# Optimization experiments

Measured on AMD Instinct MI355X. Metric: run time of the kernel, lower is better.

Reference implementation:

```python
import jax, jax.numpy as jnp
import numpy as np

D_MODEL = 1024
N_HEADS = 16
HEAD = D_MODEL // N_HEADS  # 64
D_FF = 4096
LN_EPS = 1e-5


def _layernorm(x, g, b):
    mu = jnp.mean(x, axis=-1, keepdims=True)
    var = jnp.mean(jnp.square(x - mu), axis=-1, keepdims=True)
    return (x - mu) * jax.lax.rsqrt(var + LN_EPS) * g + b


def _mha(q_in, k_in, v_in, Wq, Wk, Wv, bv, causal):
    # Wq/Wk/Wv: [H, d_model, head]; bv: [H, head] (value proj has bias, q/k do not)
    q = jnp.einsum('bsd,hde->bhse', q_in, Wq)
    k = jnp.einsum('btd,hde->bhte', k_in, Wk)
    v = jnp.einsum('btd,hde->bhte', v_in, Wv) + bv[None, :, None, :]
    scale = HEAD ** -0.5
    scores = jnp.einsum('bhse,bhte->bhst', q, k) * scale
    if causal:
        S, T = scores.shape[-2], scores.shape[-1]
        mask = jnp.tril(jnp.ones((S, T), dtype=bool))
        scores = jnp.where(mask, scores, -jnp.inf)
    p = jax.nn.softmax(scores, axis=-1)
    o = jnp.einsum('bhst,bhte->bhse', p, v)  # [B,H,S,head]
    B, H, S, E = o.shape
    return o.transpose(0, 2, 1, 3).reshape(B, S, H * E)  # concat heads in order


def setup_inputs() -> dict:
    key = jax.random.key(0)
    ks = jax.random.split(key, 20)
    B, S, T = 2, 2048, 2048
    sd = D_MODEL ** -0.5
    inp = {
        'input_tensor': jax.random.normal(ks[0], (B, S, D_MODEL), jnp.float32),
        'encoder_output': jax.random.normal(ks[1], (B, T, D_MODEL), jnp.float32),
        # masked self-attention params
        'Wq1': jax.random.normal(ks[2], (N_HEADS, D_MODEL, HEAD), jnp.float32) * sd,
        'Wk1': jax.random.normal(ks[3], (N_HEADS, D_MODEL, HEAD), jnp.float32) * sd,
        'Wv1': jax.random.normal(ks[4], (N_HEADS, D_MODEL, HEAD), jnp.float32) * sd,
        'bv1': jnp.zeros((N_HEADS, HEAD), jnp.float32),
        # cross-attention params
        'Wq2': jax.random.normal(ks[5], (N_HEADS, D_MODEL, HEAD), jnp.float32) * sd,
        'Wk2': jax.random.normal(ks[6], (N_HEADS, D_MODEL, HEAD), jnp.float32) * sd,
        'Wv2': jax.random.normal(ks[7], (N_HEADS, D_MODEL, HEAD), jnp.float32) * sd,
        'bv2': jnp.zeros((N_HEADS, HEAD), jnp.float32),
        # layernorms
        'g1': jnp.ones((D_MODEL,), jnp.float32), 'be1': jnp.zeros((D_MODEL,), jnp.float32),
        'g2': jnp.ones((D_MODEL,), jnp.float32), 'be2': jnp.zeros((D_MODEL,), jnp.float32),
        'g3': jnp.ones((D_MODEL,), jnp.float32), 'be3': jnp.zeros((D_MODEL,), jnp.float32),
        # FFN
        'Wf1': jax.random.normal(ks[8], (D_MODEL, D_FF), jnp.float32) * sd,
        'bf1': jnp.zeros((D_FF,), jnp.float32),
        'Wf2': jax.random.normal(ks[9], (D_FF, D_MODEL), jnp.float32) * (D_FF ** -0.5),
        'bf2': jnp.zeros((D_MODEL,), jnp.float32),
    }
    return inp


def reference(input_tensor, encoder_output, Wq1, Wk1, Wv1, bv1, Wq2, Wk2, Wv2, bv2,
              g1, be1, g2, be2, g3, be3, Wf1, bf1, Wf2, bf2):
    x = input_tensor
    # masked (causal) self-attention; dropout is identity in eval
    sa = _mha(x, x, x, Wq1, Wk1, Wv1, bv1, causal=True)
    x = _layernorm(sa + input_tensor, g1, be1)
    # cross-attention with encoder output (no mask)
    ca = _mha(x, encoder_output, encoder_output, Wq2, Wk2, Wv2, bv2, causal=False)
    x = _layernorm(x + ca, g2, be2)
    # FFN
    ffn = jax.nn.relu(x @ Wf1 + bf1) @ Wf2 + bf2
    x = _layernorm(x + ffn, g3, be3)
    return x
```

## Files before the change

kernel.cpp:

```cpp
#include <hip/hip_runtime.h>
#include <stdint.h>
#include <stddef.h>
#include <type_traits>

typedef __attribute__((ext_vector_type(8))) short short8;
typedef __attribute__((ext_vector_type(4))) short short4_t;
typedef __attribute__((ext_vector_type(4))) float float4_t;
typedef __attribute__((ext_vector_type(4))) unsigned uint4_t;

#define DEV static __device__ __forceinline__

#define QSCALE 0.18033688011112042f

DEV short f2bf(float f) {
  unsigned u = __builtin_bit_cast(unsigned, f);
  u = (u + 0x7FFFu + ((u >> 16) & 1u)) >> 16;
  return (short)(unsigned short)u;
}

DEV void load_lds16(const short* g, short* l) {
  __builtin_amdgcn_global_load_lds((const __attribute__((address_space(1))) void*)g,
                                   (__attribute__((address_space(3))) void*)l,
                                   16, 0, 0);
}

__global__ __launch_bounds__(256) void transpose_cvt(const float* __restrict__ src,
                                                     short* __restrict__ dst,
                                                     int R, int C) {
  __shared__ float t[64][65];
  src += (size_t)blockIdx.z * R * C;
  dst += (size_t)blockIdx.z * R * C;
  const int tid = threadIdx.x;
  const int r0 = blockIdx.y * 64, c0 = blockIdx.x * 64;
#pragma unroll
  for (int i = 0; i < 16; i++) {
    int r = i * 4 + (tid >> 6);
    t[r][tid & 63] = src[(size_t)(r0 + r) * C + c0 + (tid & 63)];
  }
  __syncthreads();
#pragma unroll
  for (int i = 0; i < 16; i++) {
    int c = i * 4 + (tid >> 6);
    dst[(size_t)(c0 + c) * R + r0 + (tid & 63)] = f2bf(t[tid & 63][c]);
  }
}

struct Repack6 {
  const float* src[6];
  short* dst[6];
};
__global__ __launch_bounds__(256) void transpose_cvt6(Repack6 a) {
  __shared__ float t[64][65];
  const int mat = blockIdx.z >> 4;
  const int head = blockIdx.z & 15;
  const float* src = a.src[mat] + (size_t)head * 1024 * 64;
  short* dst = a.dst[mat] + (size_t)head * 64 * 1024;
  const int tid = threadIdx.x;
  const int r0 = blockIdx.y * 64;
#pragma unroll
  for (int i = 0; i < 16; i++) {
    int r = i * 4 + (tid >> 6);
    t[r][tid & 63] = src[(size_t)(r0 + r) * 64 + (tid & 63)];
  }
  __syncthreads();
#pragma unroll
  for (int i = 0; i < 16; i++) {
    int c = i * 4 + (tid >> 6);
    dst[(size_t)c * 1024 + r0 + (tid & 63)] = f2bf(t[tid & 63][c]);
  }
}

__global__ __launch_bounds__(256) void cvt_bf16_2(const float* __restrict__ inA,
                                                  short* __restrict__ outA,
                                                  const float* __restrict__ inB,
                                                  short* __restrict__ outB, int n4) {
  int i = blockIdx.x * 256 + threadIdx.x;
  const float* in = blockIdx.z ? inB : inA;
  short* out = blockIdx.z ? outB : outA;
  if (i < n4) {
    float4_t v = ((const float4_t*)in)[i];
    short4_t o;
    o.x = f2bf(v.x); o.y = f2bf(v.y); o.z = f2bf(v.z); o.w = f2bf(v.w);
    ((short4_t*)out)[i] = o;
  }
}

struct GemmArgs {
  const short* A;
  const short* Bt;
  int M, N, K;
  float* outf;
  short* outb;
  short* Qo;
  short* Ko;
  short* Vt;
  const float* bias;
};

template <int MODE>
DEV void scatter1(const GemmArgs& args, int row, int col, float v) {
  if constexpr (MODE == 0) {
    int sel = col >> 10, cc = col & 1023;
    int h = cc >> 6, e = cc & 63;
    int b_ = row >> 11, s = row & 2047;
    if (sel == 0)
      args.Qo[(((size_t)(b_ * 16 + h)) * 2048 + s) * 64 + e] = f2bf(v * QSCALE);
    else if (sel == 1)
      args.Ko[(((size_t)(b_ * 16 + h)) * 2048 + s) * 64 + e] = f2bf(v);
    else {
      v += args.bias[cc];
      args.Vt[(((size_t)(b_ * 16 + h)) * 64 + e) * 2048 + s] = f2bf(v);
    }
  } else if constexpr (MODE == 1) {
    int h = col >> 6, e = col & 63;
    int b_ = row >> 11, s = row & 2047;
    args.Qo[(((size_t)(b_ * 16 + h)) * 2048 + s) * 64 + e] = f2bf(v * QSCALE);
  } else if constexpr (MODE == 2) {
    int sel = col >> 10, cc = col & 1023;
    int h = cc >> 6, e = cc & 63;
    int b_ = row >> 11, s = row & 2047;
    if (sel == 0)
      args.Ko[(((size_t)(b_ * 16 + h)) * 2048 + s) * 64 + e] = f2bf(v);
    else {
      v += args.bias[cc];
      args.Vt[(((size_t)(b_ * 16 + h)) * 64 + e) * 2048 + s] = f2bf(v);
    }
  } else if constexpr (MODE == 3) {
    v += args.bias[col];
    v = v > 0.f ? v : 0.f;
    args.outb[(size_t)row * args.N + col] = f2bf(v);
  } else {
    v += args.bias[col];
    args.outf[(size_t)row * args.N + col] = v;
  }
}

template <int MODE>
__global__ __launch_bounds__(256) void gemm_k(GemmArgs args) {
  constexpr int BM = 128, BK = 64;
  __shared__ short As[2][BM * BK];
  __shared__ short Bs[2][BM * BK];
  const int tid = threadIdx.x;
  const int lane = tid & 63;
  const int w = tid >> 6;
  const int wr = w >> 1, wc = w & 1;

  const int nwgx = gridDim.x;
  const int nxy = nwgx * gridDim.y;
  const int nwg = nxy * gridDim.z;
  const int orig = (blockIdx.z * gridDim.y + blockIdx.y) * nwgx + blockIdx.x;
  const int q8 = nwg >> 3;
  const int swz = (orig & 7) * q8 + (orig >> 3);
  const int zsl = swz / nxy;
  const int xy = swz % nxy;
  const int row0 = (xy / nwgx) * BM;
  const int col0 = (xy % nwgx) * BM;

  const int K = args.K;
  const int kLen = K / gridDim.z;
  const int kbase = zsl * kLen;
  const short* Ab = args.A + (size_t)row0 * K;
  const short* Bb = args.Bt + (size_t)col0 * K;
  float4_t acc[4][4] = {};
  const int r = lane & 15, kg = lane >> 4, rx = r & 7;

  auto stage = [&](int buf, int k0) {
#pragma unroll
    for (int i = 0; i < 4; i++) {
      int c = i * 256 + tid;
      int rw = c >> 3, sc = (c & 7) ^ (rw & 7);
      load_lds16(Ab + (size_t)rw * K + k0 + sc * 8, &As[buf][c * 8]);
    }
#pragma unroll
    for (int i = 0; i < 4; i++) {
      int c = i * 256 + tid;
      int rw = c >> 3, sc = (c & 7) ^ (rw & 7);
      load_lds16(Bb + (size_t)rw * K + k0 + sc * 8, &Bs[buf][c * 8]);
    }
  };

  stage(0, kbase);
  __syncthreads();
  int buf = 0;
  const int nk = kLen / BK;
  for (int t = 0; t < nk; t++) {
    if (t + 1 < nk) stage(buf ^ 1, kbase + (t + 1) * BK);
#pragma unroll
    for (int kk = 0; kk < BK; kk += 32) {
      const int ch = kk >> 3;
      short8 a[4], b[4];
#pragma unroll
      for (int m = 0; m < 4; m++)
        a[m] = *(const short8*)&As[buf][(wr * 64 + m * 16 + r) * BK + ((ch + kg) ^ rx) * 8];
#pragma unroll
      for (int n = 0; n < 4; n++)
        b[n] = *(const short8*)&Bs[buf][(wc * 64 + n * 16 + r) * BK + ((ch + kg) ^ rx) * 8];
#pragma unroll
      for (int m = 0; m < 4; m++)
#pragma unroll
        for (int n = 0; n < 4; n++)
          acc[m][n] = __builtin_amdgcn_mfma_f32_16x16x32_bf16(a[m], b[n], acc[m][n], 0, 0, 0);
    }
    __syncthreads();
    buf ^= 1;
  }

  float* dst5 = args.outf + (size_t)zsl * args.M * args.N;
#pragma unroll
  for (int m = 0; m < 4; m++)
#pragma unroll
    for (int n = 0; n < 4; n++)
#pragma unroll
      for (int j = 0; j < 4; j++) {
        int row = row0 + wr * 64 + m * 16 + kg * 4 + j;
        int col = col0 + wc * 64 + n * 16 + r;
        if constexpr (MODE == 5)
          dst5[(size_t)row * args.N + col] = acc[m][n][j];
        else
          scatter1<MODE>(args, row, col, acc[m][n][j]);
      }
}

template <int MODE>
__global__ __launch_bounds__(512, 2) void gemm256_k(GemmArgs args) {
  extern __shared__ short lds[];
  const int tid = threadIdx.x;
  const int lane = tid & 63;
  const int w = tid >> 6;
  const int wr = w >> 2, wc = w & 3;

  const int nwgx = gridDim.x;
  const int nwg = nwgx * gridDim.y;
  const int orig = blockIdx.y * nwgx + blockIdx.x;
  const int q8 = nwg >> 3;
  const int swz = (orig & 7) * q8 + (orig >> 3);
  const int row0 = (swz / nwgx) * 256;
  const int col0 = (swz % nwgx) * 256;

  const int K = args.K;
  const short* Ab = args.A + (size_t)row0 * K;
  const short* Bb = args.Bt + (size_t)col0 * K;
  const int r = lane & 15, kg = lane >> 4, rx = r & 7;
  float4_t acc[8][4] = {};

  auto stage = [&](int buf, int k0) {
    short* Ad = lds + buf * 16384;
    short* Bd = lds + 32768 + buf * 16384;
#pragma unroll
    for (int i = 0; i < 4; i++) {
      int c = i * 512 + tid;
      int rw = c >> 3, sc = (c & 7) ^ (rw & 7);
      load_lds16(Ab + (size_t)rw * K + k0 + sc * 8, Ad + c * 8);
    }
#pragma unroll
    for (int i = 0; i < 4; i++) {
      int c = i * 512 + tid;
      int rw = c >> 3, sc = (c & 7) ^ (rw & 7);
      load_lds16(Bb + (size_t)rw * K + k0 + sc * 8, Bd + c * 8);
    }
  };

  stage(0, 0);
  __syncthreads();
  int buf = 0;
  const int nk = K / 64;
  for (int t = 0; t < nk; t++) {
    if (t + 1 < nk) stage(buf ^ 1, (t + 1) * 64);
    const short* Ar = lds + buf * 16384;
    const short* Br = lds + 32768 + buf * 16384;
#pragma unroll
    for (int kk = 0; kk < 64; kk += 32) {
      const int ch = kk >> 3;
      short8 a[8], b[4];
#pragma unroll
      for (int m = 0; m < 8; m++)
        a[m] = *(const short8*)&Ar[(wr * 128 + m * 16 + r) * 64 + ((ch + kg) ^ rx) * 8];
#pragma unroll
      for (int n = 0; n < 4; n++)
        b[n] = *(const short8*)&Br[(wc * 64 + n * 16 + r) * 64 + ((ch + kg) ^ rx) * 8];
#pragma unroll
      for (int m = 0; m < 8; m++)
#pragma unroll
        for (int n = 0; n < 4; n++)
          acc[m][n] = __builtin_amdgcn_mfma_f32_16x16x32_bf16(a[m], b[n], acc[m][n], 0, 0, 0);
    }
    __syncthreads();
    buf ^= 1;
  }

#pragma unroll
  for (int m = 0; m < 8; m++)
#pragma unroll
    for (int n = 0; n < 4; n++)
#pragma unroll
      for (int j = 0; j < 4; j++)
        scatter1<MODE>(args, row0 + wr * 128 + m * 16 + kg * 4 + j,
                       col0 + wc * 64 + n * 16 + r, acc[m][n][j]);
}

template <bool CAUSAL>
__global__ __launch_bounds__(256) void attn_k(const short* __restrict__ Q,
                                              const short* __restrict__ Kq,
                                              const short* __restrict__ Vt,
                                              float* __restrict__ Out) {
  __shared__ short kst[2][64 * 64];
  __shared__ short vst[2][64 * 64];
  __shared__ unsigned p_lds[4][32 * 32];
  const int tid = threadIdx.x;
  const int lane = tid & 63;
  const int w = tid >> 6;
  const int bh = blockIdx.y;
  const int b_ = bh >> 4, h = bh & 15;
  const int qb = (blockIdx.x + blockIdx.y) & 15;
  const int qt = (blockIdx.y & 16) ? (15 - qb) : qb;
  const int q0w = qt * 128 + w * 32;
  const int r = lane & 15, kg = lane >> 4;
  const int rx = r & 7;
  const size_t base = (size_t)bh * 2048 * 64;
  const short* Qb = Q + base;
  const short* Kb = Kq + base;
  const short* Vb = Vt + base;

  short8 q[2][2];
#pragma unroll
  for (int qg = 0; qg < 2; qg++)
#pragma unroll
    for (int half = 0; half < 2; half++)
      q[qg][half] = *(const short8*)&Qb[(size_t)(q0w + qg * 16 + r) * 64 + half * 32 + kg * 8];

  float4_t o[2][4] = {};
  float lp[2] = {0.f, 0.f};

  const int NT = CAUSAL ? 2 * qt + 2 : 32;
  const float4_t zero4 = {0.f, 0.f, 0.f, 0.f};

  const int c0 = tid, c1 = tid + 256;
  const int row0s = c0 >> 3, cc0 = (c0 & 7) ^ (row0s & 7);
  const int row1s = c1 >> 3, cc1 = (c1 & 7) ^ (row1s & 7);

  auto stage = [&](int buf, int kt) {
    const short* ktk = Kb + (size_t)kt * 64 * 64;
    const short* ktv = Vb + (size_t)kt * 64;
    load_lds16(ktk + row0s * 64 + cc0 * 8, &kst[buf][c0 * 8]);
    load_lds16(ktk + row1s * 64 + cc1 * 8, &kst[buf][c1 * 8]);
    load_lds16(ktv + (size_t)row0s * 2048 + cc0 * 8, &vst[buf][c0 * 8]);
    load_lds16(ktv + (size_t)row1s * 2048 + cc1 * 8, &vst[buf][c1 * 8]);
  };

  auto body = [&](auto BUFC, int kt) {
    constexpr int BUF = decltype(BUFC)::value;
    short8 kb[4][2];
#pragma unroll
    for (int grp = 0; grp < 4; grp++)
#pragma unroll
      for (int half = 0; half < 2; half++)
        kb[grp][half] = *(const short8*)&kst[BUF][(grp * 16 + r) * 64 + ((half * 4 + kg) ^ rx) * 8];

    unsigned* p32 = &p_lds[w][0];
#pragma unroll
    for (int qg = 0; qg < 2; qg++) {
      float4_t sc[4];
      __builtin_amdgcn_s_setprio(1);
#pragma unroll
      for (int grp = 0; grp < 4; grp++) {
        float4_t t0 = __builtin_amdgcn_mfma_f32_16x16x32_bf16(kb[grp][0], q[qg][0], zero4, 0, 0, 0);
        sc[grp] = __builtin_amdgcn_mfma_f32_16x16x32_bf16(kb[grp][1], q[qg][1], t0, 0, 0, 0);
      }
      __builtin_amdgcn_s_setprio(0);

      float s[16];
#pragma unroll
      for (int grp = 0; grp < 4; grp++)
#pragma unroll
        for (int j = 0; j < 4; j++) s[grp * 4 + j] = sc[grp][j];

      if (CAUSAL && kt >= 2 * qt) {
        const int qrow = q0w + qg * 16 + r;
#pragma unroll
        for (int grp = 0; grp < 4; grp++)
#pragma unroll
          for (int j = 0; j < 4; j++)
            if (kt * 64 + grp * 16 + kg * 4 + j > qrow) s[grp * 4 + j] = -1e30f;
      }

      float p[16];
      float ps = 0.f;
#pragma unroll
      for (int i = 0; i < 16; i++) {
        p[i] = __builtin_amdgcn_exp2f(s[i]);
        ps += p[i];
      }
      lp[qg] += ps;

#pragma unroll
      for (int grp = 0; grp < 4; grp++) {
        unsigned pk01, pk23;
        asm("v_cvt_pk_bf16_f32 %0, %1, %2" : "=v"(pk01) : "v"(p[grp * 4 + 0]), "v"(p[grp * 4 + 1]));
        asm("v_cvt_pk_bf16_f32 %0, %1, %2" : "=v"(pk23) : "v"(p[grp * 4 + 2]), "v"(p[grp * 4 + 3]));
        int idx = (qg * 16 + r) * 32 + ((2 * grp + (kg >> 1)) ^ rx) * 4 + (kg & 1) * 2;
        p32[idx] = pk01;
        p32[idx + 1] = pk23;
      }
    }
    __builtin_amdgcn_sched_barrier(0);

    short8 pa[2][2];
#pragma unroll
    for (int qg = 0; qg < 2; qg++)
#pragma unroll
      for (int half = 0; half < 2; half++) {
        const int db = (qg * 16 + r) * 32 + ((half * 4 + kg) ^ rx) * 4;
        uint4_t t;
        t.x = p32[db + 0];
        t.y = p32[db + 1];
        t.z = p32[db + 2];
        t.w = p32[db + 3];
        pa[qg][half] = __builtin_bit_cast(short8, t);
      }

    __builtin_amdgcn_s_setprio(1);
#pragma unroll
    for (int n = 0; n < 4; n++) {
      short8 v0 = *(const short8*)&vst[BUF][(n * 16 + r) * 64 + ((0 * 4 + kg) ^ rx) * 8];
      short8 v1 = *(const short8*)&vst[BUF][(n * 16 + r) * 64 + ((1 * 4 + kg) ^ rx) * 8];
#pragma unroll
      for (int qg = 0; qg < 2; qg++) {
        o[qg][n] = __builtin_amdgcn_mfma_f32_16x16x32_bf16(v0, pa[qg][0], o[qg][n], 0, 0, 0);
        o[qg][n] = __builtin_amdgcn_mfma_f32_16x16x32_bf16(v1, pa[qg][1], o[qg][n], 0, 0, 0);
      }
    }
    __builtin_amdgcn_s_setprio(0);
  };

  stage(0, 0);
  __syncthreads();

  for (int kt = 0; kt < NT; kt += 2) {
    if (kt + 1 < NT) stage(1, kt + 1);
    body(std::integral_constant<int, 0>{}, kt);
    __syncthreads();
    if (kt + 1 >= NT) break;
    if (kt + 2 < NT) stage(0, kt + 2);
    body(std::integral_constant<int, 1>{}, kt + 1);
    __syncthreads();
  }

#pragma unroll
  for (int qg = 0; qg < 2; qg++) {
    float l = lp[qg];
    l += __shfl_xor(l, 16);
    l += __shfl_xor(l, 32);
    const float inv = 1.0f / l;
    float* orow = Out + ((size_t)b_ * 2048 + q0w + qg * 16 + r) * 1024 + h * 64;
#pragma unroll
    for (int n = 0; n < 4; n++)
#pragma unroll
      for (int j = 0; j < 4; j++)
        orow[n * 16 + kg * 4 + j] = o[qg][n][j] * inv;
  }
}

__global__ __launch_bounds__(256) void add_ln_k(const float* __restrict__ X,
                                                const float* __restrict__ Y,
                                                const float* __restrict__ g,
                                                const float* __restrict__ be,
                                                float* __restrict__ outf,
                                                short* __restrict__ outb) {
  __shared__ float red[8];
  const int row = blockIdx.x;
  const int t = threadIdx.x;
  const int lane = t & 63, w = t >> 6;
  float4_t v = ((const float4_t*)(X + (size_t)row * 1024))[t];
  float4_t u = ((const float4_t*)(Y + (size_t)row * 1024))[t];
  v.x += u.x; v.y += u.y; v.z += u.z; v.w += u.w;
  float s = v.x + v.y + v.z + v.w;
#pragma unroll
  for (int off = 32; off >= 1; off >>= 1) s += __shfl_xor(s, off);
  if (lane == 0) red[w] = s;
  __syncthreads();
  float mean = (red[0] + red[1] + red[2] + red[3]) * (1.f / 1024.f);
  float dx = v.x - mean, dy = v.y - mean, dz = v.z - mean, dw = v.w - mean;
  float q2 = dx * dx + dy * dy + dz * dz + dw * dw;
#pragma unroll
  for (int off = 32; off >= 1; off >>= 1) q2 += __shfl_xor(q2, off);
  if (lane == 0) red[4 + w] = q2;
  __syncthreads();
  float var = (red[4] + red[5] + red[6] + red[7]) * (1.f / 1024.f);
  float rs = rsqrtf(var + 1e-5f);
  float4_t gg = ((const float4_t*)g)[t];
  float4_t bb = ((const float4_t*)be)[t];
  float4_t o;
  o.x = dx * rs * gg.x + bb.x;
  o.y = dy * rs * gg.y + bb.y;
  o.z = dz * rs * gg.z + bb.z;
  o.w = dw * rs * gg.w + bb.w;
  ((float4_t*)(outf + (size_t)row * 1024))[t] = o;
  if (outb != nullptr) {
    short4_t ob;
    ob.x = f2bf(o.x); ob.y = f2bf(o.y); ob.z = f2bf(o.z); ob.w = f2bf(o.w);
    ((short4_t*)(outb + (size_t)row * 1024))[t] = ob;
  }
}

__global__ __launch_bounds__(256) void add_ln2_k(const float* __restrict__ X,
                                                 const float* __restrict__ P0,
                                                 const float* __restrict__ P1,
                                                 const float* __restrict__ bias,
                                                 const float* __restrict__ g,
                                                 const float* __restrict__ be,
                                                 float* __restrict__ outf) {
  __shared__ float red[8];
  const int row = blockIdx.x;
  const int t = threadIdx.x;
  const int lane = t & 63, w = t >> 6;
  float4_t v = ((const float4_t*)(X + (size_t)row * 1024))[t];
  float4_t u0 = ((const float4_t*)(P0 + (size_t)row * 1024))[t];
  float4_t u1 = ((const float4_t*)(P1 + (size_t)row * 1024))[t];
  float4_t bi = ((const float4_t*)bias)[t];
  v.x += u0.x + u1.x + bi.x;
  v.y += u0.y + u1.y + bi.y;
  v.z += u0.z + u1.z + bi.z;
  v.w += u0.w + u1.w + bi.w;
  float s = v.x + v.y + v.z + v.w;
#pragma unroll
  for (int off = 32; off >= 1; off >>= 1) s += __shfl_xor(s, off);
  if (lane == 0) red[w] = s;
  __syncthreads();
  float mean = (red[0] + red[1] + red[2] + red[3]) * (1.f / 1024.f);
  float dx = v.x - mean, dy = v.y - mean, dz = v.z - mean, dw = v.w - mean;
  float q2 = dx * dx + dy * dy + dz * dz + dw * dw;
#pragma unroll
  for (int off = 32; off >= 1; off >>= 1) q2 += __shfl_xor(q2, off);
  if (lane == 0) red[4 + w] = q2;
  __syncthreads();
  float var = (red[4] + red[5] + red[6] + red[7]) * (1.f / 1024.f);
  float rs = rsqrtf(var + 1e-5f);
  float4_t gg = ((const float4_t*)g)[t];
  float4_t bb = ((const float4_t*)be)[t];
  float4_t o;
  o.x = dx * rs * gg.x + bb.x;
  o.y = dy * rs * gg.y + bb.y;
  o.z = dz * rs * gg.z + bb.z;
  o.w = dw * rs * gg.w + bb.w;
  ((float4_t*)(outf + (size_t)row * 1024))[t] = o;
}

extern "C" void kernel_launch(void* const* d_in, const int* in_sizes, int n_in,
                              void* d_out, int out_size, void* d_ws, size_t ws_size,
                              hipStream_t stream) {
  (void)in_sizes; (void)n_in; (void)out_size; (void)ws_size;
  const float* x_in = (const float*)d_in[0];
  const float* enc  = (const float*)d_in[1];
  const float* Wq1  = (const float*)d_in[2];
  const float* Wk1  = (const float*)d_in[3];
  const float* Wv1  = (const float*)d_in[4];
  const float* bv1  = (const float*)d_in[5];
  const float* Wq2  = (const float*)d_in[6];
  const float* Wk2  = (const float*)d_in[7];
  const float* Wv2  = (const float*)d_in[8];
  const float* bv2  = (const float*)d_in[9];
  const float* g1   = (const float*)d_in[10];
  const float* be1  = (const float*)d_in[11];
  const float* g2   = (const float*)d_in[12];
  const float* be2  = (const float*)d_in[13];
  const float* g3   = (const float*)d_in[14];
  const float* be3  = (const float*)d_in[15];
  const float* Wf1  = (const float*)d_in[16];
  const float* bf1  = (const float*)d_in[17];
  const float* Wf2  = (const float*)d_in[18];
  const float* bf2  = (const float*)d_in[19];
  float* out = (float*)d_out;

  (void)hipFuncSetAttribute((const void*)gemm256_k<0>,
                            hipFuncAttributeMaxDynamicSharedMemorySize, 131072);
  (void)hipFuncSetAttribute((const void*)gemm256_k<3>,
                            hipFuncAttributeMaxDynamicSharedMemorySize, 131072);

  char* ws = (char*)d_ws;
  size_t off = 0;
  auto alloc = [&](size_t bytes) -> void* {
    void* p = ws + off;
    off += (bytes + 255) & ~(size_t)255;
    return p;
  };
  short* wqkv1t = (short*)alloc((size_t)3072 * 1024 * 2);
  short* wq2t   = (short*)alloc((size_t)1024 * 1024 * 2);
  short* wkv2t  = (short*)alloc((size_t)2048 * 1024 * 2);
  short* wf1t   = (short*)alloc((size_t)4096 * 1024 * 2);
  short* wf2t   = (short*)alloc((size_t)1024 * 4096 * 2);
  short* act_bf = (short*)alloc((size_t)4096 * 1024 * 2);
  short* enc_bf = (short*)alloc((size_t)4096 * 1024 * 2);
  short* Qb     = (short*)alloc((size_t)4096 * 1024 * 2);
  short* Kb     = (short*)alloc((size_t)4096 * 1024 * 2);
  short* Vtb    = (short*)alloc((size_t)4096 * 1024 * 2);
  float* tmp_f  = (float*)alloc((size_t)4096 * 1024 * 4);
  float* xbuf   = (float*)alloc((size_t)4096 * 1024 * 4);
  short* h_bf   = (short*)alloc((size_t)4096 * 4096 * 2);
  float* pbuf   = (float*)alloc((size_t)2 * 4096 * 1024 * 4);

  dim3 blk(256);
  dim3 blk5(512);
  Repack6 rp;
  rp.src[0] = Wq1; rp.dst[0] = wqkv1t;
  rp.src[1] = Wk1; rp.dst[1] = wqkv1t + 1024 * 1024;
  rp.src[2] = Wv1; rp.dst[2] = wqkv1t + 2 * 1024 * 1024;
  rp.src[3] = Wq2; rp.dst[3] = wq2t;
  rp.src[4] = Wk2; rp.dst[4] = wkv2t;
  rp.src[5] = Wv2; rp.dst[5] = wkv2t + 1024 * 1024;
  transpose_cvt6<<<dim3(1, 16, 96), blk, 0, stream>>>(rp);
  transpose_cvt<<<dim3(64, 16, 1), blk, 0, stream>>>(Wf1, wf1t, 1024, 4096);
  transpose_cvt<<<dim3(16, 64, 1), blk, 0, stream>>>(Wf2, wf2t, 4096, 1024);
  cvt_bf16_2<<<dim3(4096, 1, 2), blk, 0, stream>>>(x_in, act_bf, enc, enc_bf, 1048576);

  GemmArgs ga;
  ga.A = act_bf; ga.Bt = wqkv1t; ga.M = 4096; ga.N = 3072; ga.K = 1024;
  ga.outf = nullptr; ga.outb = nullptr; ga.Qo = Qb; ga.Ko = Kb; ga.Vt = Vtb; ga.bias = bv1;
  gemm256_k<0><<<dim3(12, 16), blk5, 131072, stream>>>(ga);
  attn_k<true><<<dim3(16, 32), blk, 0, stream>>>(Qb, Kb, Vtb, tmp_f);
  add_ln_k<<<4096, blk, 0, stream>>>(tmp_f, x_in, g1, be1, xbuf, act_bf);

  ga.A = act_bf; ga.Bt = wq2t; ga.M = 4096; ga.N = 1024; ga.K = 1024;
  ga.Qo = Qb; ga.Ko = nullptr; ga.Vt = nullptr; ga.bias = nullptr;
  gemm_k<1><<<dim3(8, 32), blk, 0, stream>>>(ga);
  ga.A = enc_bf; ga.Bt = wkv2t; ga.M = 4096; ga.N = 2048; ga.K = 1024;
  ga.Qo = nullptr; ga.Ko = Kb; ga.Vt = Vtb; ga.bias = bv2;
  gemm_k<2><<<dim3(16, 32), blk, 0, stream>>>(ga);
  attn_k<false><<<dim3(16, 32), blk, 0, stream>>>(Qb, Kb, Vtb, tmp_f);
  add_ln_k<<<4096, blk, 0, stream>>>(xbuf, tmp_f, g2, be2, xbuf, act_bf);

  ga.A = act_bf; ga.Bt = wf1t; ga.M = 4096; ga.N = 4096; ga.K = 1024;
  ga.outb = h_bf; ga.bias = bf1; ga.Qo = nullptr; ga.Ko = nullptr; ga.Vt = nullptr;
  gemm256_k<3><<<dim3(16, 16), blk5, 131072, stream>>>(ga);
  ga.A = h_bf; ga.Bt = wf2t; ga.M = 4096; ga.N = 1024; ga.K = 4096;
  ga.outf = pbuf; ga.outb = nullptr; ga.bias = nullptr;
  gemm_k<5><<<dim3(8, 32, 2), blk, 0, stream>>>(ga);
  add_ln2_k<<<4096, blk, 0, stream>>>(xbuf, pbuf, pbuf + (size_t)4096 * 1024,
                                      bf2, g3, be3, out);
}
```

Measured before the change: 338.5 us.

## Split 256-tile GEMM K-tiles into half stages with fine-grained vmcnt pipelining

The 256x256 GEMM now stages each 64-wide K tile as two 32-wide halves in separate LDS slots and prefetches up to two half-tiles ahead. Explicit s_waitcnt vmcnt levels and raw s_barrier calls replace the single full __syncthreads per tile, so loads overlap with MFMA work more finely. MFMA blocks are wrapped in s_setprio to favour math issue. The cost is more barriers per tile and hand-managed wait counts that rely on the compiler's load ordering.

```diff
diff --git a/kernel.cpp b/kernel.cpp
--- a/kernel.cpp
+++ b/kernel.cpp
@@ -222,7 +222,7 @@
 }
 
 template <int MODE>
-__global__ __launch_bounds__(512, 2) void gemm256_k(GemmArgs args) {
+__global__ __launch_bounds__(512, 2) void gemm256p_k(GemmArgs args) {
   extern __shared__ short lds[];
   const int tid = threadIdx.x;
   const int lane = tid & 63;
@@ -240,52 +240,80 @@
   const int K = args.K;
   const short* Ab = args.A + (size_t)row0 * K;
   const short* Bb = args.Bt + (size_t)col0 * K;
-  const int r = lane & 15, kg = lane >> 4, rx = r & 7;
+  const int r = lane & 15, kg = lane >> 4, rx3 = r & 3;
   float4_t acc[8][4] = {};
 
-  auto stage = [&](int buf, int k0) {
-    short* Ad = lds + buf * 16384;
-    short* Bd = lds + 32768 + buf * 16384;
-#pragma unroll
-    for (int i = 0; i < 4; i++) {
+  auto stageHalf = [&](int slot, const short* base, int k0) {
+    short* dst = lds + slot * 8192;
+#pragma unroll
+    for (int i = 0; i < 2; i++) {
       int c = i * 512 + tid;
-      int rw = c >> 3, sc = (c & 7) ^ (rw & 7);
-      load_lds16(Ab + (size_t)rw * K + k0 + sc * 8, Ad + c * 8);
-    }
-#pragma unroll
-    for (int i = 0; i < 4; i++) {
-      int c = i * 512 + tid;
-      int rw = c >> 3, sc = (c & 7) ^ (rw & 7);
-      load_lds16(Bb + (size_t)rw * K + k0 + sc * 8, Bd + c * 8);
+      int rw = c >> 2, sc = (c & 3) ^ (rw & 3);
+      load_lds16(base + (size_t)rw * K + k0 + sc * 8, dst + c * 8);
     }
   };
 
-  stage(0, 0);
-  __syncthreads();
-  int buf = 0;
-  const int nk = K / 64;
-  for (int t = 0; t < nk; t++) {
-    if (t + 1 < nk) stage(buf ^ 1, (t + 1) * 64);
-    const short* Ar = lds + buf * 16384;
-    const short* Br = lds + 32768 + buf * 16384;
-#pragma unroll
-    for (int kk = 0; kk < 64; kk += 32) {
-      const int ch = kk >> 3;
-      short8 a[8], b[4];
-#pragma unroll
-      for (int m = 0; m < 8; m++)
-        a[m] = *(const short8*)&Ar[(wr * 128 + m * 16 + r) * 64 + ((ch + kg) ^ rx) * 8];
+  auto compute = [&](int t, int ks) {
+    const short* As = lds + ((t & 1) * 4 + ks) * 8192;
+    const short* Bs = lds + ((t & 1) * 4 + 2 + ks) * 8192;
+    short8 a[8], b[4];
+#pragma unroll
+    for (int m = 0; m < 8; m++)
+      a[m] = *(const short8*)&As[(wr * 128 + m * 16 + r) * 32 + (kg ^ rx3) * 8];
+#pragma unroll
+    for (int n = 0; n < 4; n++)
+      b[n] = *(const short8*)&Bs[(wc * 64 + n * 16 + r) * 32 + (kg ^ rx3) * 8];
+    __builtin_amdgcn_s_setprio(1);
+#pragma unroll
+    for (int m = 0; m < 8; m++)
 #pragma unroll
       for (int n = 0; n < 4; n++)
-        b[n] = *(const short8*)&Br[(wc * 64 + n * 16 + r) * 64 + ((ch + kg) ^ rx) * 8];
-#pragma unroll
-      for (int m = 0; m < 8; m++)
-#pragma unroll
-        for (int n = 0; n < 4; n++)
-          acc[m][n] = __builtin_amdgcn_mfma_f32_16x16x32_bf16(a[m], b[n], acc[m][n], 0, 0, 0);
-    }
-    __syncthreads();
-    buf ^= 1;
+        acc[m][n] = __builtin_amdgcn_mfma_f32_16x16x32_bf16(a[m], b[n], acc[m][n], 0, 0, 0);
+    __builtin_amdgcn_s_setprio(0);
+  };
+
+  auto waitv = [&](int cnt) {
+    if (cnt >= 8) asm volatile("s_waitcnt vmcnt(8)" ::: "memory");
+    else if (cnt == 4) asm volatile("s_waitcnt vmcnt(4)" ::: "memory");
+    else asm volatile("s_waitcnt vmcnt(0)" ::: "memory");
+  };
+
+  const int nt = K / 64;
+  stageHalf(0, Ab, 0);
+  stageHalf(2, Bb, 0);
+  stageHalf(1, Ab, 32);
+  stageHalf(3, Bb, 32);
+  if (nt > 1) { stageHalf(4, Ab, 64); stageHalf(6, Bb, 64); }
+  int prev = (nt > 1) ? 4 : 0;
+
+  for (int t = 0; t < nt; t++) {
+    int cur = 0;
+    if (t + 1 < nt) {
+      stageHalf(((t + 1) & 1) * 4 + 1, Ab, (t + 1) * 64 + 32);
+      stageHalf(((t + 1) & 1) * 4 + 3, Bb, (t + 1) * 64 + 32);
+      cur = 4;
+    }
+    waitv(cur + prev);
+    __builtin_amdgcn_s_barrier();
+    __builtin_amdgcn_sched_barrier(0);
+    compute(t, 0);
+    asm volatile("" ::: "memory");
+    __builtin_amdgcn_s_barrier();
+    prev = cur;
+
+    cur = 0;
+    if (t + 2 < nt) {
+      stageHalf((t & 1) * 4 + 0, Ab, (t + 2) * 64);
+      stageHalf((t & 1) * 4 + 2, Bb, (t + 2) * 64);
+      cur = 4;
+    }
+    waitv(cur + prev);
+    __builtin_amdgcn_s_barrier();
+    __builtin_amdgcn_sched_barrier(0);
+    compute(t, 1);
+    asm volatile("" ::: "memory");
+    __builtin_amdgcn_s_barrier();
+    prev = cur;
   }
 
 #pragma unroll
@@ -571,9 +599,9 @@
   const float* bf2  = (const float*)d_in[19];
   float* out = (float*)d_out;
 
-  (void)hipFuncSetAttribute((const void*)gemm256_k<0>,
+  (void)hipFuncSetAttribute((const void*)gemm256p_k<0>,
                             hipFuncAttributeMaxDynamicSharedMemorySize, 131072);
-  (void)hipFuncSetAttribute((const void*)gemm256_k<3>,
+  (void)hipFuncSetAttribute((const void*)gemm256p_k<3>,
                             hipFuncAttributeMaxDynamicSharedMemorySize, 131072);
 
   char* ws = (char*)d_ws;
@@ -615,7 +643,7 @@
   GemmArgs ga;
   ga.A = act_bf; ga.Bt = wqkv1t; ga.M = 4096; ga.N = 3072; ga.K = 1024;
   ga.outf = nullptr; ga.outb = nullptr; ga.Qo = Qb; ga.Ko = Kb; ga.Vt = Vtb; ga.bias = bv1;
-  gemm256_k<0><<<dim3(12, 16), blk5, 131072, stream>>>(ga);
+  gemm256p_k<0><<<dim3(12, 16), blk5, 131072, stream>>>(ga);
   attn_k<true><<<dim3(16, 32), blk, 0, stream>>>(Qb, Kb, Vtb, tmp_f);
   add_ln_k<<<4096, blk, 0, stream>>>(tmp_f, x_in, g1, be1, xbuf, act_bf);
 
@@ -630,7 +658,7 @@
 
   ga.A = act_bf; ga.Bt = wf1t; ga.M = 4096; ga.N = 4096; ga.K = 1024;
   ga.outb = h_bf; ga.bias = bf1; ga.Qo = nullptr; ga.Ko = nullptr; ga.Vt = nullptr;
-  gemm256_k<3><<<dim3(16, 16), blk5, 131072, stream>>>(ga);
+  gemm256p_k<3><<<dim3(16, 16), blk5, 131072, stream>>>(ga);
   ga.A = h_bf; ga.Bt = wf2t; ga.M = 4096; ga.N = 1024; ga.K = 4096;
   ga.outf = pbuf; ga.outb = nullptr; ga.bias = nullptr;
   gemm_k<5><<<dim3(8, 32, 2), blk, 0, stream>>>(ga);
```

Result: slower. 350.8 us (+3.6%).
